# Performance work log

Hardware: AMD Instinct MI355X
Metric: run time of the kernel (lower is better)

## Reference

```python
import jax, jax.numpy as jnp
import numpy as np

N, M, D = 32768, 8192, 256


def setup_inputs() -> dict:
    key = jax.random.key(0)
    kx, ky = jax.random.split(key)
    inputDataX = jax.random.normal(kx, (N, D), dtype=jnp.float32)
    targetDataY = jax.random.normal(ky, (M, D), dtype=jnp.float32)
    dualVariablePsi = jnp.zeros((M,), dtype=jnp.float32)
    return {"inputDataX": inputDataX, "targetDataY": targetDataY, "dualVariablePsi": dualVariablePsi}


def reference(inputDataX, targetDataY, dualVariablePsi):
    # cost[i,j] = 0.5 * ||x_i - y_j||^2, built GEMM-style as in the torch module
    sq_x = jnp.sum(inputDataX ** 2, axis=1, keepdims=True)          # [N, 1]
    sq_y = jnp.sum(targetDataY ** 2, axis=1)[None, :]               # [1, M]
    cross = inputDataX @ targetDataY.T                              # [N, M]
    cost = (sq_x + sq_y - 2.0 * cross) * 0.5
    row_min = jnp.min(cost - dualVariablePsi[None, :], axis=1)      # [N]
    n = inputDataX.shape[0]
    return jnp.sum(row_min) / n + jnp.mean(dualVariablePsi)
```

## Files before the change

### kernel.cpp

```cpp
#include <hip/hip_runtime.h>
#include <hip/hip_bf16.h>
#include <stdint.h>

#define NROWS 32768
#define MCOLS 8192
#define DDIM  256

#define BM 128
#define BN 128
#define NT (MCOLS/BN)
#define NWG (NROWS/BM)

typedef __attribute__((ext_vector_type(8))) int   int8v;
typedef __attribute__((ext_vector_type(4))) int   int4v;
typedef __attribute__((ext_vector_type(4))) float f32x4;

__device__ __forceinline__ uint32_t pk4_fp8(float4 v) {
  int p = __builtin_amdgcn_cvt_pk_fp8_f32(v.x, v.y, 0, false);
  p = __builtin_amdgcn_cvt_pk_fp8_f32(v.z, v.w, p, true);
  return (uint32_t)p;
}
__device__ __forceinline__ uint32_t fkey(float f) {
  uint32_t b = __float_as_uint(f);
  return (b & 0x80000000u) ? ~b : (b | 0x80000000u);
}
__device__ __forceinline__ float funkey(uint32_t k) {
  uint32_t b = (k & 0x80000000u) ? (k ^ 0x80000000u) : ~k;
  return __uint_as_float(b);
}
__device__ __forceinline__ f32x4 vmin4(f32x4 x, f32x4 y) {
  f32x4 r;
  r[0] = fminf(x[0], y[0]); r[1] = fminf(x[1], y[1]);
  r[2] = fminf(x[2], y[2]); r[3] = fminf(x[3], y[3]);
  return r;
}

__global__ void k_prep(const float* __restrict__ X, const float* __restrict__ Y,
                       const float* __restrict__ psi,
                       uint32_t* __restrict__ Xq, uint32_t* __restrict__ Yq,
                       float* __restrict__ xhalf, float* __restrict__ cbuf,
                       uint32_t* __restrict__ rowkey, float* __restrict__ sum_accum)
{
  const int lane = threadIdx.x & 63;
  const int gw = (blockIdx.x * blockDim.x + threadIdx.x) >> 6;
  const int nw = (gridDim.x * blockDim.x) >> 6;
  for (int row = gw; row < NROWS + MCOLS; row += nw) {
    const bool isX = row < NROWS;
    const int r = isX ? row : row - NROWS;
    const float* src = isX ? (X + (size_t)row * DDIM) : (Y + (size_t)r * DDIM);
    float4 v = ((const float4*)src)[lane];
    const uint32_t pk = pk4_fp8(v);
    if (isX) Xq[(size_t)row * 64 + lane] = pk;
    else     Yq[(size_t)r   * 64 + lane] = pk;
    float s = v.x*v.x + v.y*v.y + v.z*v.z + v.w*v.w;
    #pragma unroll
    for (int m = 32; m >= 1; m >>= 1) s += __shfl_xor(s, m);
    if (lane == 0) {
      if (isX) { xhalf[row] = 0.5f * s; rowkey[row] = 0xFFFFFFFFu; }
      else     { cbuf[r] = 0.5f * s - psi[r]; }
    }
  }
  if (blockIdx.x == 0 && threadIdx.x == 0) sum_accum[0] = 0.0f;
}

#define STAGEB(t_, nb_) do {                                                    \
    _Pragma("unroll") for (int _g = 0; _g < 4; ++_g) {                          \
      const int _row = _g * 32 + wid * 4 + (lane >> 4);                         \
      const char* _src = (const char*)Yq + (size_t)((t_) * BN + _row) * 256     \
                         + ((((lane & 15) ^ (_row & 15)) << 4));                \
      __builtin_amdgcn_global_load_lds(                                         \
          (const __attribute__((address_space(1))) uint32_t*)_src,              \
          (__attribute__((address_space(3))) uint32_t*)                         \
              (ldsB + (nb_) * 32768 + (_g * 32 + wid * 4) * 256), 16, 0, 0);    \
    }                                                                           \
  } while (0)

#define RB16(n_, kc_, h_)                                                       \
  (*(const int4v*)(bRd + ((wc * 32 + (n_) * 16 + c15) << 8) +                   \
                   ((((kc_) * 8 + w4 * 2 + (h_)) ^ c15) << 4)))

__global__ __attribute__((amdgpu_flat_work_group_size(512, 512),
                          amdgpu_waves_per_eu(2, 2)))
void k_gemm(const uint32_t* __restrict__ Xq, const uint32_t* __restrict__ Yq,
            const float* __restrict__ cbuf, uint32_t* __restrict__ rowkey)
{
  __shared__ __align__(16) char ldsB[2 * 32768];

  const int brow = blockIdx.x * BM;
  const int tid  = threadIdx.x;
  const int wid  = tid >> 6;
  const int lane = tid & 63;
  const int wr = wid >> 2;
  const int wc = wid & 3;
  const int c15 = lane & 15;
  const int w4  = lane >> 4;

  int8v a[4][2];
  {
    const char* aBase = (const char*)Xq + ((size_t)(brow + wr * 64 + c15) << 8) + w4 * 32;
    #pragma unroll
    for (int m = 0; m < 4; ++m)
      #pragma unroll
      for (int kc = 0; kc < 2; ++kc)
        a[m][kc] = *(const int8v*)(aBase + m * 16 * 256 + kc * 128);
  }

  STAGEB(0, 0);
  asm volatile("s_waitcnt vmcnt(0)" ::: "memory");
  __builtin_amdgcn_s_barrier();

  f32x4 vmin[4];
  #pragma unroll
  for (int m = 0; m < 4; ++m)
    vmin[m] = (f32x4){3.4e38f, 3.4e38f, 3.4e38f, 3.4e38f};

  #pragma unroll 1
  for (int t = 0; t < NT; ++t) {
    const int buf = t & 1;
    const char* bRd = ldsB + buf * 32768;

    const float cj0 = cbuf[t * BN + wc * 32 +  0 + c15];
    const float cj1 = cbuf[t * BN + wc * 32 + 16 + c15];

    if (t + 1 < NT) STAGEB(t + 1, buf ^ 1);

    int8v bf[2][2];
    #pragma unroll
    for (int n = 0; n < 2; ++n)
      #pragma unroll
      for (int kc = 0; kc < 2; ++kc) {
        const int4v lo = RB16(n, kc, 0);
        const int4v hi = RB16(n, kc, 1);
        bf[n][kc] = (int8v){lo[0], lo[1], lo[2], lo[3], hi[0], hi[1], hi[2], hi[3]};
      }

    const f32x4 z = {0.f, 0.f, 0.f, 0.f};
    f32x4 acc[4][2];
    #pragma unroll
    for (int m = 0; m < 4; ++m) { acc[m][0] = z; acc[m][1] = z; }

    __builtin_amdgcn_s_setprio(1);
    #pragma unroll
    for (int kc = 0; kc < 2; ++kc) {
      #pragma unroll
      for (int m = 0; m < 4; ++m)
        acc[m][0] = __builtin_amdgcn_mfma_scale_f32_16x16x128_f8f6f4(
            a[m][kc], bf[0][kc], acc[m][0], 0, 0, 0, 0x7F, 0, 0x7F);
      #pragma unroll
      for (int m = 0; m < 4; ++m)
        acc[m][1] = __builtin_amdgcn_mfma_scale_f32_16x16x128_f8f6f4(
            a[m][kc], bf[1][kc], acc[m][1], 0, 0, 0, 0x7F, 0, 0x7F);
    }
    __builtin_amdgcn_s_setprio(0);

    const f32x4 c0 = {cj0, cj0, cj0, cj0};
    const f32x4 c1 = {cj1, cj1, cj1, cj1};
    #pragma unroll
    for (int m = 0; m < 4; ++m)
      vmin[m] = vmin4(vmin[m], vmin4(c0 - acc[m][0], c1 - acc[m][1]));

    asm volatile("s_waitcnt vmcnt(0)" ::: "memory");
    __builtin_amdgcn_s_barrier();
  }

  #pragma unroll
  for (int m = 0; m < 4; ++m) {
    #pragma unroll
    for (int r = 0; r < 4; ++r) {
      float v = vmin[m][r];
      v = fminf(v, __shfl_xor(v, 1));
      v = fminf(v, __shfl_xor(v, 2));
      v = fminf(v, __shfl_xor(v, 4));
      v = fminf(v, __shfl_xor(v, 8));
      vmin[m][r] = v;
    }
    if (c15 < 4) {
      float vsel = vmin[m][0];
      vsel = (c15 == 1) ? vmin[m][1] : vsel;
      vsel = (c15 == 2) ? vmin[m][2] : vsel;
      vsel = (c15 == 3) ? vmin[m][3] : vsel;
      const int row = brow + wr * 64 + m * 16 + w4 * 4 + c15;
      atomicMin((unsigned int*)&rowkey[row], fkey(vsel));
    }
  }
}

__global__ void k_rowred(const float* __restrict__ xhalf, const uint32_t* __restrict__ rowkey,
                         float* __restrict__ sum_accum)
{
  __shared__ float sh[4];
  const int i = blockIdx.x * 256 + threadIdx.x;
  float v = funkey(rowkey[i]) + xhalf[i];
  #pragma unroll
  for (int m = 32; m >= 1; m >>= 1) v += __shfl_xor(v, m);
  const int wid = threadIdx.x >> 6, lane = threadIdx.x & 63;
  if (lane == 0) sh[wid] = v;
  __syncthreads();
  if (threadIdx.x == 0) atomicAdd(sum_accum, sh[0] + sh[1] + sh[2] + sh[3]);
}

__global__ void k_final(const float* __restrict__ psi, const float* __restrict__ sum_accum,
                        float* __restrict__ out)
{
  __shared__ float sh[4];
  float s = 0.f;
  for (int i = threadIdx.x; i < MCOLS; i += 256) s += psi[i];
  #pragma unroll
  for (int m = 32; m >= 1; m >>= 1) s += __shfl_xor(s, m);
  const int wid = threadIdx.x >> 6, lane = threadIdx.x & 63;
  if (lane == 0) sh[wid] = s;
  __syncthreads();
  if (threadIdx.x == 0)
    out[0] = sum_accum[0] / (float)NROWS + (sh[0] + sh[1] + sh[2] + sh[3]) / (float)MCOLS;
}

extern "C" void kernel_launch(void* const* d_in, const int* in_sizes, int n_in,
                              void* d_out, int out_size, void* d_ws, size_t ws_size,
                              hipStream_t stream)
{
  const float* X   = (const float*)d_in[0];
  const float* Y   = (const float*)d_in[1];
  const float* psi = (const float*)d_in[2];
  float* out = (float*)d_out;

  char* ws = (char*)d_ws;
  uint32_t* Xq     = (uint32_t*)(ws);
  uint32_t* Yq     = (uint32_t*)(ws + (size_t)NROWS * DDIM);
  float* cbuf      = (float*)(ws + (size_t)(NROWS + MCOLS) * DDIM);
  uint32_t* rowkey = (uint32_t*)((char*)cbuf + (size_t)MCOLS * 4);
  float* xhalf     = (float*)((char*)rowkey + (size_t)NROWS * 4);
  float* sum_accum = (float*)((char*)xhalf + (size_t)NROWS * 4);

  k_prep  <<<2048, 256, 0, stream>>>(X, Y, psi, Xq, Yq, xhalf, cbuf, rowkey, sum_accum);
  k_gemm  <<<NWG, 512, 0, stream>>>(Xq, Yq, cbuf, rowkey);
  k_rowred<<<NROWS / 256, 256, 0, stream>>>(xhalf, rowkey, sum_accum);
  k_final <<<1, 256, 0, stream>>>(psi, sum_accum, out);
}
```

Measured before the change: 97.31 us.

## Prefetch B fragments to registers one tile ahead and stage cbuf in LDS

Restructures the GEMM main loop so that B fragments for the next tile are read from LDS into registers while the current tile's MFMAs run. Global-to-LDS staging now runs two tiles ahead, and the loop is unrolled by two with ping-pong register sets. The per-column cbuf vector is also copied once into LDS up front, so the loop no longer does global loads of it. This hides LDS read latency behind compute, at the cost of extra registers, 32KB more LDS per workgroup, and a barrier that now also waits on lgkmcnt.

```diff
diff --git a/kernel.cpp b/kernel.cpp
--- a/kernel.cpp
+++ b/kernel.cpp
@@ -75,16 +75,55 @@
     }                                                                           \
   } while (0)
 
-#define RB16(n_, kc_, h_)                                                       \
-  (*(const int4v*)(bRd + ((wc * 32 + (n_) * 16 + c15) << 8) +                   \
-                   ((((kc_) * 8 + w4 * 2 + (h_)) ^ c15) << 4)))
+#define READB(dst, buf_) do {                                                   \
+    const char* _bRd = ldsB + (buf_) * 32768;                                   \
+    _Pragma("unroll") for (int _n = 0; _n < 2; ++_n)                            \
+      _Pragma("unroll") for (int _kc = 0; _kc < 2; ++_kc) {                     \
+        const int4v _lo = *(const int4v*)(_bRd + ((wc*32 + _n*16 + c15) << 8)   \
+                          + (((_kc*8 + w4*2 + 0) ^ c15) << 4));                 \
+        const int4v _hi = *(const int4v*)(_bRd + ((wc*32 + _n*16 + c15) << 8)   \
+                          + (((_kc*8 + w4*2 + 1) ^ c15) << 4));                 \
+        dst[_n][_kc] = (int8v){_lo[0],_lo[1],_lo[2],_lo[3],                     \
+                               _hi[0],_hi[1],_hi[2],_hi[3]};                    \
+      }                                                                         \
+  } while (0)
+
+#define ITER(t_, CUR, NXT) do {                                                 \
+    asm volatile("s_waitcnt lgkmcnt(0) vmcnt(0)" ::: "memory");                 \
+    __builtin_amdgcn_s_barrier();                                               \
+    if ((t_) + 2 < NT) STAGEB((t_) + 2, (t_) & 1);                              \
+    if ((t_) + 1 < NT) READB(NXT, ((t_) + 1) & 1);                              \
+    const float cj0 = Cs[(t_) * BN + wc * 32 +  0 + c15];                       \
+    const float cj1 = Cs[(t_) * BN + wc * 32 + 16 + c15];                       \
+    const f32x4 _z = {0.f, 0.f, 0.f, 0.f};                                      \
+    f32x4 acc[4][2];                                                            \
+    _Pragma("unroll") for (int _m = 0; _m < 4; ++_m) {                          \
+      acc[_m][0] = _z; acc[_m][1] = _z;                                         \
+    }                                                                           \
+    __builtin_amdgcn_s_setprio(1);                                              \
+    _Pragma("unroll") for (int _kc = 0; _kc < 2; ++_kc) {                       \
+      _Pragma("unroll") for (int _m = 0; _m < 4; ++_m)                          \
+        acc[_m][0] = __builtin_amdgcn_mfma_scale_f32_16x16x128_f8f6f4(          \
+            a[_m][_kc], CUR[0][_kc], acc[_m][0], 0, 0, 0, 0x7F, 0, 0x7F);       \
+      _Pragma("unroll") for (int _m = 0; _m < 4; ++_m)                          \
+        acc[_m][1] = __builtin_amdgcn_mfma_scale_f32_16x16x128_f8f6f4(          \
+            a[_m][_kc], CUR[1][_kc], acc[_m][1], 0, 0, 0, 0x7F, 0, 0x7F);       \
+    }                                                                           \
+    __builtin_amdgcn_s_setprio(0);                                              \
+    const f32x4 _c0 = {cj0, cj0, cj0, cj0};                                     \
+    const f32x4 _c1 = {cj1, cj1, cj1, cj1};                                     \
+    _Pragma("unroll") for (int _m = 0; _m < 4; ++_m)                            \
+      vmin[_m] = vmin4(vmin[_m], vmin4(_c0 - acc[_m][0], _c1 - acc[_m][1]));    \
+  } while (0)
 
 __global__ __attribute__((amdgpu_flat_work_group_size(512, 512),
                           amdgpu_waves_per_eu(2, 2)))
 void k_gemm(const uint32_t* __restrict__ Xq, const uint32_t* __restrict__ Yq,
             const float* __restrict__ cbuf, uint32_t* __restrict__ rowkey)
 {
-  __shared__ __align__(16) char ldsB[2 * 32768];
+  __shared__ __align__(16) char shm[2 * 32768 + 32768];
+  char* ldsB = shm;
+  const float* Cs = (const float*)(shm + 65536);
 
   const int brow = blockIdx.x * BM;
   const int tid  = threadIdx.x;
@@ -105,62 +144,29 @@
         a[m][kc] = *(const int8v*)(aBase + m * 16 * 256 + kc * 128);
   }
 
+  #pragma unroll
+  for (int g = 0; g < 4; ++g)
+    __builtin_amdgcn_global_load_lds(
+        (const __attribute__((address_space(1))) uint32_t*)((const char*)cbuf + (g * 512 + tid) * 16),
+        (__attribute__((address_space(3))) uint32_t*)(shm + 65536 + g * 8192 + wid * 1024),
+        16, 0, 0);
   STAGEB(0, 0);
   asm volatile("s_waitcnt vmcnt(0)" ::: "memory");
   __builtin_amdgcn_s_barrier();
 
+  int8v bfA[2][2], bfB[2][2];
+  READB(bfA, 0);
+  STAGEB(1, 1);
+
   f32x4 vmin[4];
   #pragma unroll
   for (int m = 0; m < 4; ++m)
     vmin[m] = (f32x4){3.4e38f, 3.4e38f, 3.4e38f, 3.4e38f};
 
   #pragma unroll 1
-  for (int t = 0; t < NT; ++t) {
-    const int buf = t & 1;
-    const char* bRd = ldsB + buf * 32768;
-
-    const float cj0 = cbuf[t * BN + wc * 32 +  0 + c15];
-    const float cj1 = cbuf[t * BN + wc * 32 + 16 + c15];
-
-    if (t + 1 < NT) STAGEB(t + 1, buf ^ 1);
-
-    int8v bf[2][2];
-    #pragma unroll
-    for (int n = 0; n < 2; ++n)
-      #pragma unroll
-      for (int kc = 0; kc < 2; ++kc) {
-        const int4v lo = RB16(n, kc, 0);
-        const int4v hi = RB16(n, kc, 1);
-        bf[n][kc] = (int8v){lo[0], lo[1], lo[2], lo[3], hi[0], hi[1], hi[2], hi[3]};
-      }
-
-    const f32x4 z = {0.f, 0.f, 0.f, 0.f};
-    f32x4 acc[4][2];
-    #pragma unroll
-    for (int m = 0; m < 4; ++m) { acc[m][0] = z; acc[m][1] = z; }
-
-    __builtin_amdgcn_s_setprio(1);
-    #pragma unroll
-    for (int kc = 0; kc < 2; ++kc) {
-      #pragma unroll
-      for (int m = 0; m < 4; ++m)
-        acc[m][0] = __builtin_amdgcn_mfma_scale_f32_16x16x128_f8f6f4(
-            a[m][kc], bf[0][kc], acc[m][0], 0, 0, 0, 0x7F, 0, 0x7F);
-      #pragma unroll
-      for (int m = 0; m < 4; ++m)
-        acc[m][1] = __builtin_amdgcn_mfma_scale_f32_16x16x128_f8f6f4(
-            a[m][kc], bf[1][kc], acc[m][1], 0, 0, 0, 0x7F, 0, 0x7F);
-    }
-    __builtin_amdgcn_s_setprio(0);
-
-    const f32x4 c0 = {cj0, cj0, cj0, cj0};
-    const f32x4 c1 = {cj1, cj1, cj1, cj1};
-    #pragma unroll
-    for (int m = 0; m < 4; ++m)
-      vmin[m] = vmin4(vmin[m], vmin4(c0 - acc[m][0], c1 - acc[m][1]));
-
-    asm volatile("s_waitcnt vmcnt(0)" ::: "memory");
-    __builtin_amdgcn_s_barrier();
+  for (int tt = 0; tt < NT; tt += 2) {
+    ITER(tt,     bfA, bfB);
+    ITER(tt + 1, bfB, bfA);
   }
 
   #pragma unroll
```

Result: faster. 93.70 us (-3.7%).

## Stream pre-swizzled B fragments from global directly to registers, fuse row reduction

Applied to the files above, without the earlier changes.

Y is quantized into an MFMA-fragment-ordered layout so each wave loads its B operands straight from global memory into registers with double buffering, dropping the LDS staging and the per-tile barrier. X is pre-negated via the fp8 sign bit, so the bias c_j can seed the accumulator and the min is applied directly. Each wave now covers all 128 rows against 16 columns per tile. The per-row minimum is reduced in LDS and summed inside the GEMM kernel, removing the atomicMin keys and the separate row-reduction kernel. The cost is redundant global/L2 traffic for B across workgroups and more registers for A.

```diff
diff --git a/kernel.cpp b/kernel.cpp
--- a/kernel.cpp
+++ b/kernel.cpp
@@ -12,21 +12,12 @@
 #define NWG (NROWS/BM)
 
 typedef __attribute__((ext_vector_type(8))) int   int8v;
-typedef __attribute__((ext_vector_type(4))) int   int4v;
 typedef __attribute__((ext_vector_type(4))) float f32x4;
 
 __device__ __forceinline__ uint32_t pk4_fp8(float4 v) {
   int p = __builtin_amdgcn_cvt_pk_fp8_f32(v.x, v.y, 0, false);
   p = __builtin_amdgcn_cvt_pk_fp8_f32(v.z, v.w, p, true);
   return (uint32_t)p;
-}
-__device__ __forceinline__ uint32_t fkey(float f) {
-  uint32_t b = __float_as_uint(f);
-  return (b & 0x80000000u) ? ~b : (b | 0x80000000u);
-}
-__device__ __forceinline__ float funkey(uint32_t k) {
-  uint32_t b = (k & 0x80000000u) ? (k ^ 0x80000000u) : ~k;
-  return __uint_as_float(b);
 }
 __device__ __forceinline__ f32x4 vmin4(f32x4 x, f32x4 y) {
   f32x4 r;
@@ -37,9 +28,9 @@
 
 __global__ void k_prep(const float* __restrict__ X, const float* __restrict__ Y,
                        const float* __restrict__ psi,
-                       uint32_t* __restrict__ Xq, uint32_t* __restrict__ Yq,
+                       uint32_t* __restrict__ XqN, uint32_t* __restrict__ YqT,
                        float* __restrict__ xhalf, float* __restrict__ cbuf,
-                       uint32_t* __restrict__ rowkey, float* __restrict__ sum_accum)
+                       float* __restrict__ sum_accum)
 {
   const int lane = threadIdx.x & 63;
   const int gw = (blockIdx.x * blockDim.x + threadIdx.x) >> 6;
@@ -50,121 +41,95 @@
     const float* src = isX ? (X + (size_t)row * DDIM) : (Y + (size_t)r * DDIM);
     float4 v = ((const float4*)src)[lane];
     const uint32_t pk = pk4_fp8(v);
-    if (isX) Xq[(size_t)row * 64 + lane] = pk;
-    else     Yq[(size_t)r   * 64 + lane] = pk;
+    if (isX) {
+      XqN[(size_t)row * 64 + lane] = pk ^ 0x80808080u;
+    } else {
+      const int idx = (r >> 4) * 1024 + (lane >> 5) * 512 + ((lane >> 3) & 3) * 128
+                    + (r & 15) * 8 + (lane & 7);
+      YqT[idx] = pk;
+    }
     float s = v.x*v.x + v.y*v.y + v.z*v.z + v.w*v.w;
     #pragma unroll
     for (int m = 32; m >= 1; m >>= 1) s += __shfl_xor(s, m);
     if (lane == 0) {
-      if (isX) { xhalf[row] = 0.5f * s; rowkey[row] = 0xFFFFFFFFu; }
-      else     { cbuf[r] = 0.5f * s - psi[r]; }
+      if (isX) xhalf[row] = 0.5f * s;
+      else     cbuf[r] = 0.5f * s - psi[r];
     }
   }
   if (blockIdx.x == 0 && threadIdx.x == 0) sum_accum[0] = 0.0f;
 }
 
-#define STAGEB(t_, nb_) do {                                                    \
-    _Pragma("unroll") for (int _g = 0; _g < 4; ++_g) {                          \
-      const int _row = _g * 32 + wid * 4 + (lane >> 4);                         \
-      const char* _src = (const char*)Yq + (size_t)((t_) * BN + _row) * 256     \
-                         + ((((lane & 15) ^ (_row & 15)) << 4));                \
-      __builtin_amdgcn_global_load_lds(                                         \
-          (const __attribute__((address_space(1))) uint32_t*)_src,              \
-          (__attribute__((address_space(3))) uint32_t*)                         \
-              (ldsB + (nb_) * 32768 + (_g * 32 + wid * 4) * 256), 16, 0, 0);    \
-    }                                                                           \
+#define LOADB(dst, cj, t_) do {                                                 \
+    const char* _p = bBase + (size_t)(t_) * 32768;                              \
+    dst[0] = *(const int8v*)(_p);                                               \
+    dst[1] = *(const int8v*)(_p + 2048);                                        \
+    cj = cjBase[(t_) * BN];                                                     \
   } while (0)
 
-#define RB16(n_, kc_, h_)                                                       \
-  (*(const int4v*)(bRd + ((wc * 32 + (n_) * 16 + c15) << 8) +                   \
-                   ((((kc_) * 8 + w4 * 2 + (h_)) ^ c15) << 4)))
+#define STEP(t_, CUR, cjC) do {                                                 \
+    const f32x4 _ci = {cjC, cjC, cjC, cjC};                                     \
+    f32x4 acc[8];                                                               \
+    _Pragma("unroll") for (int _m = 0; _m < 8; ++_m) acc[_m] = _ci;             \
+    __builtin_amdgcn_s_setprio(1);                                              \
+    _Pragma("unroll") for (int _m = 0; _m < 8; ++_m)                            \
+      acc[_m] = __builtin_amdgcn_mfma_scale_f32_16x16x128_f8f6f4(               \
+          a[_m][0], CUR[0], acc[_m], 0, 0, 0, 0x7F, 0, 0x7F);                   \
+    _Pragma("unroll") for (int _m = 0; _m < 8; ++_m)                            \
+      acc[_m] = __builtin_amdgcn_mfma_scale_f32_16x16x128_f8f6f4(               \
+          a[_m][1], CUR[1], acc[_m], 0, 0, 0, 0x7F, 0, 0x7F);                   \
+    __builtin_amdgcn_s_setprio(0);                                              \
+    if ((t_) + 2 < NT) LOADB(CUR, cjC, (t_) + 2);                               \
+    _Pragma("unroll") for (int _m = 0; _m < 8; ++_m)                            \
+      vmin[_m] = vmin4(vmin[_m], acc[_m]);                                      \
+  } while (0)
 
 __global__ __attribute__((amdgpu_flat_work_group_size(512, 512),
                           amdgpu_waves_per_eu(2, 2)))
-void k_gemm(const uint32_t* __restrict__ Xq, const uint32_t* __restrict__ Yq,
-            const float* __restrict__ cbuf, uint32_t* __restrict__ rowkey)
-{
-  __shared__ __align__(16) char ldsB[2 * 32768];
+void k_gemm(const uint32_t* __restrict__ XqN, const uint32_t* __restrict__ YqT,
+            const float* __restrict__ cbuf, const float* __restrict__ xhalf,
+            float* __restrict__ sum_accum)
+{
+  __shared__ float Rw[8][BM];
+  __shared__ float part[2];
 
   const int brow = blockIdx.x * BM;
   const int tid  = threadIdx.x;
   const int wid  = tid >> 6;
   const int lane = tid & 63;
-  const int wr = wid >> 2;
-  const int wc = wid & 3;
   const int c15 = lane & 15;
   const int w4  = lane >> 4;
 
-  int8v a[4][2];
+  int8v a[8][2];
   {
-    const char* aBase = (const char*)Xq + ((size_t)(brow + wr * 64 + c15) << 8) + w4 * 32;
-    #pragma unroll
-    for (int m = 0; m < 4; ++m)
+    const char* aBase = (const char*)XqN + ((size_t)(brow + c15) << 8) + w4 * 32;
+    #pragma unroll
+    for (int m = 0; m < 8; ++m)
       #pragma unroll
       for (int kc = 0; kc < 2; ++kc)
         a[m][kc] = *(const int8v*)(aBase + m * 16 * 256 + kc * 128);
   }
 
-  STAGEB(0, 0);
-  asm volatile("s_waitcnt vmcnt(0)" ::: "memory");
-  __builtin_amdgcn_s_barrier();
-
-  f32x4 vmin[4];
+  const char* bBase = (const char*)YqT + (size_t)wid * 4096 + (w4 * 16 + c15) * 32;
+  const float* cjBase = cbuf + wid * 16 + c15;
+
+  int8v bA[2], bB[2];
+  float cjA, cjB;
+  LOADB(bA, cjA, 0);
+  LOADB(bB, cjB, 1);
+
+  f32x4 vmin[8];
   #pragma unroll
-  for (int m = 0; m < 4; ++m)
+  for (int m = 0; m < 8; ++m)
     vmin[m] = (f32x4){3.4e38f, 3.4e38f, 3.4e38f, 3.4e38f};
 
   #pragma unroll 1
-  for (int t = 0; t < NT; ++t) {
-    const int buf = t & 1;
-    const char* bRd = ldsB + buf * 32768;
-
-    const float cj0 = cbuf[t * BN + wc * 32 +  0 + c15];
-    const float cj1 = cbuf[t * BN + wc * 32 + 16 + c15];
-
-    if (t + 1 < NT) STAGEB(t + 1, buf ^ 1);
-
-    int8v bf[2][2];
-    #pragma unroll
-    for (int n = 0; n < 2; ++n)
-      #pragma unroll
-      for (int kc = 0; kc < 2; ++kc) {
-        const int4v lo = RB16(n, kc, 0);
-        const int4v hi = RB16(n, kc, 1);
-        bf[n][kc] = (int8v){lo[0], lo[1], lo[2], lo[3], hi[0], hi[1], hi[2], hi[3]};
-      }
-
-    const f32x4 z = {0.f, 0.f, 0.f, 0.f};
-    f32x4 acc[4][2];
-    #pragma unroll
-    for (int m = 0; m < 4; ++m) { acc[m][0] = z; acc[m][1] = z; }
-
-    __builtin_amdgcn_s_setprio(1);
-    #pragma unroll
-    for (int kc = 0; kc < 2; ++kc) {
-      #pragma unroll
-      for (int m = 0; m < 4; ++m)
-        acc[m][0] = __builtin_amdgcn_mfma_scale_f32_16x16x128_f8f6f4(
-            a[m][kc], bf[0][kc], acc[m][0], 0, 0, 0, 0x7F, 0, 0x7F);
-      #pragma unroll
-      for (int m = 0; m < 4; ++m)
-        acc[m][1] = __builtin_amdgcn_mfma_scale_f32_16x16x128_f8f6f4(
-            a[m][kc], bf[1][kc], acc[m][1], 0, 0, 0, 0x7F, 0, 0x7F);
-    }
-    __builtin_amdgcn_s_setprio(0);
-
-    const f32x4 c0 = {cj0, cj0, cj0, cj0};
-    const f32x4 c1 = {cj1, cj1, cj1, cj1};
-    #pragma unroll
-    for (int m = 0; m < 4; ++m)
-      vmin[m] = vmin4(vmin[m], vmin4(c0 - acc[m][0], c1 - acc[m][1]));
-
-    asm volatile("s_waitcnt vmcnt(0)" ::: "memory");
-    __builtin_amdgcn_s_barrier();
+  for (int tt = 0; tt < NT; tt += 2) {
+    STEP(tt,     bA, cjA);
+    STEP(tt + 1, bB, cjB);
   }
 
   #pragma unroll
-  for (int m = 0; m < 4; ++m) {
+  for (int m = 0; m < 8; ++m) {
     #pragma unroll
     for (int r = 0; r < 4; ++r) {
       float v = vmin[m][r];
@@ -179,24 +144,23 @@
       vsel = (c15 == 1) ? vmin[m][1] : vsel;
       vsel = (c15 == 2) ? vmin[m][2] : vsel;
       vsel = (c15 == 3) ? vmin[m][3] : vsel;
-      const int row = brow + wr * 64 + m * 16 + w4 * 4 + c15;
-      atomicMin((unsigned int*)&rowkey[row], fkey(vsel));
-    }
-  }
-}
-
-__global__ void k_rowred(const float* __restrict__ xhalf, const uint32_t* __restrict__ rowkey,
-                         float* __restrict__ sum_accum)
-{
-  __shared__ float sh[4];
-  const int i = blockIdx.x * 256 + threadIdx.x;
-  float v = funkey(rowkey[i]) + xhalf[i];
-  #pragma unroll
-  for (int m = 32; m >= 1; m >>= 1) v += __shfl_xor(v, m);
-  const int wid = threadIdx.x >> 6, lane = threadIdx.x & 63;
-  if (lane == 0) sh[wid] = v;
+      Rw[wid][m * 16 + w4 * 4 + c15] = vsel;
+    }
+  }
   __syncthreads();
-  if (threadIdx.x == 0) atomicAdd(sum_accum, sh[0] + sh[1] + sh[2] + sh[3]);
+
+  float s = 0.f;
+  if (tid < BM) {
+    float rm = Rw[0][tid];
+    #pragma unroll
+    for (int w = 1; w < 8; ++w) rm = fminf(rm, Rw[w][tid]);
+    s = rm + xhalf[brow + tid];
+    #pragma unroll
+    for (int m = 32; m >= 1; m >>= 1) s += __shfl_xor(s, m);
+    if (lane == 0) part[wid] = s;
+  }
+  __syncthreads();
+  if (tid == 0) atomicAdd(sum_accum, part[0] + part[1]);
 }
 
 __global__ void k_final(const float* __restrict__ psi, const float* __restrict__ sum_accum,
@@ -224,15 +188,13 @@
   float* out = (float*)d_out;
 
   char* ws = (char*)d_ws;
-  uint32_t* Xq     = (uint32_t*)(ws);
-  uint32_t* Yq     = (uint32_t*)(ws + (size_t)NROWS * DDIM);
+  uint32_t* XqN    = (uint32_t*)(ws);
+  uint32_t* YqT    = (uint32_t*)(ws + (size_t)NROWS * DDIM);
   float* cbuf      = (float*)(ws + (size_t)(NROWS + MCOLS) * DDIM);
-  uint32_t* rowkey = (uint32_t*)((char*)cbuf + (size_t)MCOLS * 4);
-  float* xhalf     = (float*)((char*)rowkey + (size_t)NROWS * 4);
+  float* xhalf     = (float*)((char*)cbuf + (size_t)MCOLS * 4);
   float* sum_accum = (float*)((char*)xhalf + (size_t)NROWS * 4);
 
-  k_prep  <<<2048, 256, 0, stream>>>(X, Y, psi, Xq, Yq, xhalf, cbuf, rowkey, sum_accum);
-  k_gemm  <<<NWG, 512, 0, stream>>>(Xq, Yq, cbuf, rowkey);
-  k_rowred<<<NROWS / 256, 256, 0, stream>>>(xhalf, rowkey, sum_accum);
-  k_final <<<1, 256, 0, stream>>>(psi, sum_accum, out);
-}
+  k_prep <<<2048, 256, 0, stream>>>(X, Y, psi, XqN, YqT, xhalf, cbuf, sum_accum);
+  k_gemm <<<NWG, 512, 0, stream>>>(XqN, YqT, cbuf, xhalf, sum_accum);
+  k_final<<<1, 256, 0, stream>>>(psi, sum_accum, out);
+}
```

After: 180.7 us. 85.7% more time.

## Split column range across two workgroups, halve B tile, fold bias into MFMA accumulator

Applied to the files above, without the earlier changes.

Negates X in FP8 during prep so the GEMM can start each accumulator at the column bias and get c_j - x·y directly, removing the post-MFMA subtraction. The GEMM now uses 512 workgroups: each 128-row block is split over two column halves, with 64-wide B tiles in 32 KB of LDS and a 2x-unrolled double-buffered loop. Halving LDS and accumulator usage lets waves_per_eu rise to 4 for more occupancy. In exchange, each A tile is loaded twice, the number of row atomics doubles, and each tile carries more barrier overhead relative to its compute.

```diff
diff --git a/kernel.cpp b/kernel.cpp
--- a/kernel.cpp
+++ b/kernel.cpp
@@ -7,13 +7,16 @@
 #define DDIM  256
 
 #define BM 128
-#define BN 128
-#define NT (MCOLS/BN)
-#define NWG (NROWS/BM)
+#define BN 64
+#define NTT 64
+#define NWG 512
 
 typedef __attribute__((ext_vector_type(8))) int   int8v;
 typedef __attribute__((ext_vector_type(4))) int   int4v;
 typedef __attribute__((ext_vector_type(4))) float f32x4;
+
+#define AS1 __attribute__((address_space(1)))
+#define AS3 __attribute__((address_space(3)))
 
 __device__ __forceinline__ uint32_t pk4_fp8(float4 v) {
   int p = __builtin_amdgcn_cvt_pk_fp8_f32(v.x, v.y, 0, false);
@@ -37,7 +40,7 @@
 
 __global__ void k_prep(const float* __restrict__ X, const float* __restrict__ Y,
                        const float* __restrict__ psi,
-                       uint32_t* __restrict__ Xq, uint32_t* __restrict__ Yq,
+                       uint32_t* __restrict__ XqN, uint32_t* __restrict__ Yq,
                        float* __restrict__ xhalf, float* __restrict__ cbuf,
                        uint32_t* __restrict__ rowkey, float* __restrict__ sum_accum)
 {
@@ -50,8 +53,8 @@
     const float* src = isX ? (X + (size_t)row * DDIM) : (Y + (size_t)r * DDIM);
     float4 v = ((const float4*)src)[lane];
     const uint32_t pk = pk4_fp8(v);
-    if (isX) Xq[(size_t)row * 64 + lane] = pk;
-    else     Yq[(size_t)r   * 64 + lane] = pk;
+    if (isX) XqN[(size_t)row * 64 + lane] = pk ^ 0x80808080u;
+    else     Yq[(size_t)r * 64 + lane] = pk;
     float s = v.x*v.x + v.y*v.y + v.z*v.z + v.w*v.w;
     #pragma unroll
     for (int m = 32; m >= 1; m >>= 1) s += __shfl_xor(s, m);
@@ -63,49 +66,78 @@
   if (blockIdx.x == 0 && threadIdx.x == 0) sum_accum[0] = 0.0f;
 }
 
-#define STAGEB(t_, nb_) do {                                                    \
-    _Pragma("unroll") for (int _g = 0; _g < 4; ++_g) {                          \
-      const int _row = _g * 32 + wid * 4 + (lane >> 4);                         \
-      const char* _src = (const char*)Yq + (size_t)((t_) * BN + _row) * 256     \
-                         + ((((lane & 15) ^ (_row & 15)) << 4));                \
-      __builtin_amdgcn_global_load_lds(                                         \
-          (const __attribute__((address_space(1))) uint32_t*)_src,              \
-          (__attribute__((address_space(3))) uint32_t*)                         \
-              (ldsB + (nb_) * 32768 + (_g * 32 + wid * 4) * 256), 16, 0, 0);    \
+#define STAGE(t_, half_) do {                                                   \
+    __builtin_amdgcn_global_load_lds(                                           \
+        (const AS1 uint32_t*)(srcA + (size_t)(t_) * 16384),                     \
+        (AS3 uint32_t*)(ldsB + (half_) + (wid * 2 + 0) * 1024), 16, 0, 0);      \
+    __builtin_amdgcn_global_load_lds(                                           \
+        (const AS1 uint32_t*)(srcB + (size_t)(t_) * 16384),                     \
+        (AS3 uint32_t*)(ldsB + (half_) + (wid * 2 + 1) * 1024), 16, 0, 0);      \
+  } while (0)
+
+#define READBF(BUFOFF) do {                                                     \
+    _Pragma("unroll") for (int _kc = 0; _kc < 2; ++_kc) {                       \
+      const int4v _lo = *(const int4v*)(bR + (BUFOFF) +                         \
+                        (((_kc * 8 + w4 * 2 + 0) ^ c15) << 4));                 \
+      const int4v _hi = *(const int4v*)(bR + (BUFOFF) +                         \
+                        (((_kc * 8 + w4 * 2 + 1) ^ c15) << 4));                 \
+      bf[_kc] = (int8v){_lo[0],_lo[1],_lo[2],_lo[3],                            \
+                        _hi[0],_hi[1],_hi[2],_hi[3]};                           \
     }                                                                           \
   } while (0)
 
-#define RB16(n_, kc_, h_)                                                       \
-  (*(const int4v*)(bRd + ((wc * 32 + (n_) * 16 + c15) << 8) +                   \
-                   ((((kc_) * 8 + w4 * 2 + (h_)) ^ c15) << 4)))
+#define COMP(cj_) do {                                                          \
+    const f32x4 _ci = {cj_, cj_, cj_, cj_};                                     \
+    f32x4 acc[4];                                                               \
+    _Pragma("unroll") for (int _m = 0; _m < 4; ++_m) acc[_m] = _ci;             \
+    __builtin_amdgcn_s_setprio(1);                                              \
+    _Pragma("unroll") for (int _m = 0; _m < 4; ++_m)                            \
+      acc[_m] = __builtin_amdgcn_mfma_scale_f32_16x16x128_f8f6f4(               \
+          a[_m][0], bf[0], acc[_m], 0, 0, 0, 0x7F, 0, 0x7F);                    \
+    _Pragma("unroll") for (int _m = 0; _m < 4; ++_m)                            \
+      acc[_m] = __builtin_amdgcn_mfma_scale_f32_16x16x128_f8f6f4(               \
+          a[_m][1], bf[1], acc[_m], 0, 0, 0, 0x7F, 0, 0x7F);                    \
+    __builtin_amdgcn_s_setprio(0);                                              \
+    _Pragma("unroll") for (int _m = 0; _m < 4; ++_m)                            \
+      vmin[_m] = vmin4(vmin[_m], acc[_m]);                                      \
+  } while (0)
 
 __global__ __attribute__((amdgpu_flat_work_group_size(512, 512),
-                          amdgpu_waves_per_eu(2, 2)))
-void k_gemm(const uint32_t* __restrict__ Xq, const uint32_t* __restrict__ Yq,
+                          amdgpu_waves_per_eu(4, 4)))
+void k_gemm(const uint32_t* __restrict__ XqN, const uint32_t* __restrict__ Yq,
             const float* __restrict__ cbuf, uint32_t* __restrict__ rowkey)
 {
-  __shared__ __align__(16) char ldsB[2 * 32768];
-
-  const int brow = blockIdx.x * BM;
+  __shared__ __align__(16) char ldsB[2 * 16384];
+
+  const int brow = (blockIdx.x >> 1) * BM;
+  const int bcol = (blockIdx.x & 1) * (MCOLS / 2);
   const int tid  = threadIdx.x;
   const int wid  = tid >> 6;
   const int lane = tid & 63;
-  const int wr = wid >> 2;
-  const int wc = wid & 3;
+  const int rg    = wid >> 2;
+  const int strip = wid & 3;
   const int c15 = lane & 15;
   const int w4  = lane >> 4;
 
   int8v a[4][2];
   {
-    const char* aBase = (const char*)Xq + ((size_t)(brow + wr * 64 + c15) << 8) + w4 * 32;
+    const char* aBase = (const char*)XqN + ((size_t)(brow + rg * 64 + c15) << 8) + w4 * 32;
     #pragma unroll
     for (int m = 0; m < 4; ++m)
       #pragma unroll
       for (int kc = 0; kc < 2; ++kc)
-        a[m][kc] = *(const int8v*)(aBase + m * 16 * 256 + kc * 128);
-  }
-
-  STAGEB(0, 0);
+        a[m][kc] = *(const int8v*)(aBase + m * 4096 + kc * 128);
+  }
+
+  const int cA = wid * 8 + w4;
+  const int cB = cA + 4;
+  const char* srcA = (const char*)Yq + (size_t)(bcol + cA) * 256 + ((c15 ^ (cA & 15)) << 4);
+  const char* srcB = (const char*)Yq + (size_t)(bcol + cB) * 256 + ((c15 ^ (cB & 15)) << 4);
+  const char* bR = ldsB + (strip * 16 + c15) * 256;
+  const float* cjPtr = cbuf + bcol + strip * 16 + c15;
+
+  STAGE(0, 0);
+  float cjA = cjPtr[0], cjB;
   asm volatile("s_waitcnt vmcnt(0)" ::: "memory");
   __builtin_amdgcn_s_barrier();
 
@@ -114,51 +146,21 @@
   for (int m = 0; m < 4; ++m)
     vmin[m] = (f32x4){3.4e38f, 3.4e38f, 3.4e38f, 3.4e38f};
 
+  int8v bf[2];
   #pragma unroll 1
-  for (int t = 0; t < NT; ++t) {
-    const int buf = t & 1;
-    const char* bRd = ldsB + buf * 32768;
-
-    const float cj0 = cbuf[t * BN + wc * 32 +  0 + c15];
-    const float cj1 = cbuf[t * BN + wc * 32 + 16 + c15];
-
-    if (t + 1 < NT) STAGEB(t + 1, buf ^ 1);
-
-    int8v bf[2][2];
-    #pragma unroll
-    for (int n = 0; n < 2; ++n)
-      #pragma unroll
-      for (int kc = 0; kc < 2; ++kc) {
-        const int4v lo = RB16(n, kc, 0);
-        const int4v hi = RB16(n, kc, 1);
-        bf[n][kc] = (int8v){lo[0], lo[1], lo[2], lo[3], hi[0], hi[1], hi[2], hi[3]};
-      }
-
-    const f32x4 z = {0.f, 0.f, 0.f, 0.f};
-    f32x4 acc[4][2];
-    #pragma unroll
-    for (int m = 0; m < 4; ++m) { acc[m][0] = z; acc[m][1] = z; }
-
-    __builtin_amdgcn_s_setprio(1);
-    #pragma unroll
-    for (int kc = 0; kc < 2; ++kc) {
-      #pragma unroll
-      for (int m = 0; m < 4; ++m)
-        acc[m][0] = __builtin_amdgcn_mfma_scale_f32_16x16x128_f8f6f4(
-            a[m][kc], bf[0][kc], acc[m][0], 0, 0, 0, 0x7F, 0, 0x7F);
-      #pragma unroll
-      for (int m = 0; m < 4; ++m)
-        acc[m][1] = __builtin_amdgcn_mfma_scale_f32_16x16x128_f8f6f4(
-            a[m][kc], bf[1][kc], acc[m][1], 0, 0, 0, 0x7F, 0, 0x7F);
-    }
-    __builtin_amdgcn_s_setprio(0);
-
-    const f32x4 c0 = {cj0, cj0, cj0, cj0};
-    const f32x4 c1 = {cj1, cj1, cj1, cj1};
-    #pragma unroll
-    for (int m = 0; m < 4; ++m)
-      vmin[m] = vmin4(vmin[m], vmin4(c0 - acc[m][0], c1 - acc[m][1]));
-
+  for (int tt = 0; tt < NTT; tt += 2) {
+    STAGE(tt + 1, 16384);
+    cjB = cjPtr[(tt + 1) * 64];
+    READBF(0);
+    COMP(cjA);
+    asm volatile("s_waitcnt vmcnt(0)" ::: "memory");
+    __builtin_amdgcn_s_barrier();
+    if (tt + 2 < NTT) {
+      STAGE(tt + 2, 0);
+      cjA = cjPtr[(tt + 2) * 64];
+    }
+    READBF(16384);
+    COMP(cjB);
     asm volatile("s_waitcnt vmcnt(0)" ::: "memory");
     __builtin_amdgcn_s_barrier();
   }
@@ -179,7 +181,7 @@
       vsel = (c15 == 1) ? vmin[m][1] : vsel;
       vsel = (c15 == 2) ? vmin[m][2] : vsel;
       vsel = (c15 == 3) ? vmin[m][3] : vsel;
-      const int row = brow + wr * 64 + m * 16 + w4 * 4 + c15;
+      const int row = brow + rg * 64 + m * 16 + w4 * 4 + c15;
       atomicMin((unsigned int*)&rowkey[row], fkey(vsel));
     }
   }
@@ -224,15 +226,15 @@
   float* out = (float*)d_out;
 
   char* ws = (char*)d_ws;
-  uint32_t* Xq     = (uint32_t*)(ws);
+  uint32_t* XqN    = (uint32_t*)(ws);
   uint32_t* Yq     = (uint32_t*)(ws + (size_t)NROWS * DDIM);
   float* cbuf      = (float*)(ws + (size_t)(NROWS + MCOLS) * DDIM);
   uint32_t* rowkey = (uint32_t*)((char*)cbuf + (size_t)MCOLS * 4);
   float* xhalf     = (float*)((char*)rowkey + (size_t)NROWS * 4);
   float* sum_accum = (float*)((char*)xhalf + (size_t)NROWS * 4);
 
-  k_prep  <<<2048, 256, 0, stream>>>(X, Y, psi, Xq, Yq, xhalf, cbuf, rowkey, sum_accum);
-  k_gemm  <<<NWG, 512, 0, stream>>>(Xq, Yq, cbuf, rowkey);
+  k_prep  <<<2048, 256, 0, stream>>>(X, Y, psi, XqN, Yq, xhalf, cbuf, rowkey, sum_accum);
+  k_gemm  <<<NWG, 512, 0, stream>>>(XqN, Yq, cbuf, rowkey);
   k_rowred<<<NROWS / 256, 256, 0, stream>>>(xhalf, rowkey, sum_accum);
   k_final <<<1, 256, 0, stream>>>(psi, sum_accum, out);
 }
```

Result: slower. 143.1 us (+47.1%).
